# Kernel optimization log

Hardware: AMD Instinct MI355X
Metric: run time of the kernel (lower is better)

Reference implementation:

```python
import jax, jax.numpy as jnp
import numpy as np

N_NODES = 10000
N_EDGES = 320000
MUL = 32            # multiplicity of each irrep block (32x0e + 32x1o)
H = 4               # attention heads (divides MUL)
D_IN = MUL + 3 * MUL  # 128
N_BASIS = 8         # radial basis size (edge_scalar_attr dim)
HID = 64            # features=[64] hidden layer of the weight-MLP
INV3 = 1.0 / np.sqrt(3.0)  # CG normalization for 1o x 1o -> 0e


def _mlp(x, w1, b1, w2):
    # HTensorProductMLP weight net: edge scalars -> per-path uvu weights
    h = jax.nn.gelu(x @ w1 * (1.0 / np.sqrt(N_BASIS)) + b1)
    return (h @ w2) * (1.0 / np.sqrt(HID))  # (E, 4*MUL)


def _tp_uvu(w, xs, xv, ys, yv):
    # uvu tensor product of (32x0e+32x1o) x (1x0e+1x1o) keeping {0e,1o} outputs.
    # Sorted output blocks: [0e: s*s, 0e: v.v, 1o: s*v, 1o: v*s]
    w = w.reshape(-1, 4, MUL)
    o0 = w[:, 0] * xs * ys[:, None]                              # (E,MUL)
    o1 = w[:, 1] * jnp.einsum('eud,ed->eu', xv, yv) * INV3       # (E,MUL)
    o2 = w[:, 2][:, :, None] * xs[:, :, None] * yv[:, None, :]   # (E,MUL,3)
    o3 = w[:, 3][:, :, None] * xv * ys[:, None, None]            # (E,MUL,3)
    return o0, o1, o2, o3


def setup_inputs() -> dict:
    key = jax.random.key(0)
    ks = jax.random.split(key, 13)
    E, N = N_EDGES, N_NODES
    return {
        'edge_src': jax.random.randint(ks[0], (E,), 0, N, dtype=jnp.int32),
        'edge_dst': jax.random.randint(ks[1], (E,), 0, N, dtype=jnp.int32),
        'edge_scalar_attr': jax.random.uniform(ks[2], (E, N_BASIS), dtype=jnp.float32),
        'edge_attr': jax.random.normal(ks[3], (E, 4), dtype=jnp.float32),
        'edge_weight_cutoff': jax.random.uniform(ks[4], (E,), dtype=jnp.float32),
        'node_f': jax.random.normal(ks[5], (N, D_IN), dtype=jnp.float32),
        'wk1': jax.random.normal(ks[6], (N_BASIS, HID), dtype=jnp.float32),
        'bk1': jnp.zeros((HID,), jnp.float32),
        'wk2': jax.random.normal(ks[7], (HID, 4 * MUL), dtype=jnp.float32),
        'wv1': jax.random.normal(ks[8], (N_BASIS, HID), dtype=jnp.float32),
        'bv1': jnp.zeros((HID,), jnp.float32),
        'wv2': jax.random.normal(ks[9], (HID, 4 * MUL), dtype=jnp.float32),
        'W_dot': jax.random.normal(ks[10], (4, H, MUL, MUL), dtype=jnp.float32),
        'W_lin_s': jax.random.normal(ks[11], (2 * MUL, MUL), dtype=jnp.float32),
        'W_lin_v': jax.random.normal(ks[12], (2 * MUL, MUL), dtype=jnp.float32),
    }


def reference(edge_src, edge_dst, edge_scalar_attr, edge_attr, edge_weight_cutoff,
              node_f, wk1, bk1, wk2, wv1, bv1, wv2, W_dot, W_lin_s, W_lin_v):
    N = node_f.shape[0]
    xs = node_f[:, :MUL]                       # (N,MUL)   0e block
    xv = node_f[:, MUL:].reshape(N, MUL, 3)    # (N,MUL,3) 1o block
    ys = edge_attr[:, 0]                       # (E,)  Y_0
    yv = edge_attr[:, 1:4]                     # (E,3) Y_1
    sxs, sxv = xs[edge_src], xv[edge_src]      # gather source node feats

    # keys: per-edge equivariant tensor-product MLP
    wk = _mlp(edge_scalar_attr, wk1, bk1, wk2)
    k0, k1, kv0, kv1 = _tp_uvu(wk, sxs, sxv, ys, yv)

    # attention logits: fully-connected TP (dst node, key) -> Hx0e
    qs, qv = xs[edge_dst], xv[edge_dst]
    inv_fan = 1.0 / np.sqrt(4.0 * MUL * MUL)
    d = (jnp.einsum('huv,eu,ev->eh', W_dot[0], qs, k0)
         + jnp.einsum('huv,eu,ev->eh', W_dot[1], qs, k1)
         + jnp.einsum('huv,eud,evd->eh', W_dot[2], qv, kv0) * INV3
         + jnp.einsum('huv,eud,evd->eh', W_dot[3], qv, kv1) * INV3) * inv_fan
    expw = edge_weight_cutoff[:, None] * jnp.exp(d)              # (E,H)
    z = jax.ops.segment_sum(expw, edge_dst, num_segments=N)      # (N,H)
    z = jnp.where(z == 0.0, 1.0, z)
    alpha = expw / z[edge_dst]                                   # (E,H)

    # values: second per-edge equivariant tensor-product MLP
    wv = _mlp(edge_scalar_attr, wv1, bv1, wv2)
    v0, v1, vv0, vv1 = _tp_uvu(wv, sxs, sxv, ys, yv)
    sa = jnp.sqrt(jax.nn.relu(alpha))                            # (E,H)
    Ee = sa.shape[0]
    m = MUL // H
    e0 = (v0.reshape(Ee, H, m) * sa[:, :, None]).reshape(Ee, MUL)
    e1 = (v1.reshape(Ee, H, m) * sa[:, :, None]).reshape(Ee, MUL)
    e2 = (vv0.reshape(Ee, H, m, 3) * sa[:, :, None, None]).reshape(Ee, 3 * MUL)
    e3 = (vv1.reshape(Ee, H, m, 3) * sa[:, :, None, None]).reshape(Ee, 3 * MUL)
    edge_v = jnp.concatenate([e0, e1, e2, e3], axis=-1)          # (E, 8*MUL)

    agg = jax.ops.segment_sum(edge_v, edge_dst, num_segments=N)  # (N, 8*MUL)

    # equivariant HLinear: mix multiplicities within each irrep
    s = agg[:, :2 * MUL]                                         # (N,2*MUL)
    v = agg[:, 2 * MUL:].reshape(N, 2 * MUL, 3)                  # (N,2*MUL,3)
    inv_l = 1.0 / np.sqrt(2.0 * MUL)
    out_s = (s @ W_lin_s) * inv_l                                # (N,MUL)
    out_v = jnp.einsum('nud,uw->nwd', v, W_lin_v) * inv_l        # (N,MUL,3)
    return jnp.concatenate([out_s, out_v.reshape(N, 3 * MUL)], axis=-1)
```

## Files before the change

### kernel.cpp

```cpp
#include <hip/hip_runtime.h>


constexpr float INV3    = 0.57735026918962576f;
constexpr float INV_SQ8 = 0.35355339059327373f;
constexpr float INV_HID = 0.125f;
constexpr float INV_FAN = 0.015625f;
constexpr float INV_L   = 0.125f;
constexpr int   MAXD    = 128;

__device__ __forceinline__ float gelu_tanh(float x) {
  float u = 0.7978845608028654f * (x + 0.044715f * x * x * x);
  float e = __expf(2.0f * u);
  return x * (1.0f - 1.0f / (e + 1.0f));
}

__global__ void k_zero(int* __restrict__ p, int n) {
  int i = blockIdx.x * 256 + threadIdx.x;
  if (i < n) p[i] = 0;
}

__global__ void k_hist(const int* __restrict__ dst, int* __restrict__ cnt, int E) {
  int e = blockIdx.x * 256 + threadIdx.x;
  if (e < E) atomicAdd(&cnt[dst[e]], 1);
}

__global__ __launch_bounds__(256) void k_scan(const int* __restrict__ cnt,
                                              int* __restrict__ rowptr, int N) {
  __shared__ int wsum[4];
  __shared__ int woff[4];
  __shared__ int carry;
  int t = threadIdx.x, wave = t >> 6, lane = t & 63;
  if (t == 0) { carry = 0; rowptr[0] = 0; }
  __syncthreads();
  for (int base = 0; base < N; base += 256) {
    int i = base + t;
    int inc = (i < N) ? cnt[i] : 0;
#pragma unroll
    for (int off = 1; off < 64; off <<= 1) {
      int y = __shfl_up(inc, off, 64);
      if (lane >= off) inc += y;
    }
    if (lane == 63) wsum[wave] = inc;
    __syncthreads();
    if (t == 0) {
      int r = 0;
      for (int w = 0; w < 4; w++) { woff[w] = r; r += wsum[w]; }
    }
    __syncthreads();
    int incl = inc + woff[wave] + carry;
    if (i < N) rowptr[i + 1] = incl;
    __syncthreads();
    if (t == 255) carry = incl;
    __syncthreads();
  }
}

__global__ void k_fill(const int* __restrict__ dst, const int* __restrict__ rowptr,
                       int* __restrict__ cursor, int* __restrict__ csr, int E) {
  int e = blockIdx.x * 256 + threadIdx.x;
  if (e < E) {
    int d = dst[e];
    int s = atomicAdd(&cursor[d], 1);
    csr[rowptr[d] + s] = e;
  }
}

__global__ void k_dhist(const int* __restrict__ rowptr, int* __restrict__ dbin, int N) {
  int n = blockIdx.x * 256 + threadIdx.x;
  if (n < N) {
    int deg = rowptr[n + 1] - rowptr[n];
    atomicAdd(&dbin[min(deg, 127)], 1);
  }
}

__global__ void k_dscan(const int* __restrict__ dbin, int* __restrict__ doff) {
  if (threadIdx.x == 0 && blockIdx.x == 0) {
    int r = 0;
    for (int d = 127; d >= 0; --d) { doff[d] = r; r += dbin[d]; }
  }
}

__global__ void k_dfill(const int* __restrict__ rowptr, const int* __restrict__ doff,
                        int* __restrict__ dcur, int* __restrict__ nperm, int N) {
  int n = blockIdx.x * 256 + threadIdx.x;
  if (n < N) {
    int d = min(rowptr[n + 1] - rowptr[n], 127);
    int p = doff[d] + atomicAdd(&dcur[d], 1);
    nperm[p] = n;
  }
}

__global__ __launch_bounds__(256) void k_gather(
    const int* __restrict__ csr, const int* __restrict__ esrc,
    const float* __restrict__ xattr, const float* __restrict__ eattr,
    const float* __restrict__ cutoff,
    float* __restrict__ xc, float* __restrict__ ec, float* __restrict__ cc,
    int* __restrict__ srcc, int E) {
  int p = blockIdx.x * 256 + threadIdx.x;
  if (p >= E) return;
  int e = csr[p];
  srcc[p] = esrc[e];
  cc[p] = cutoff[e];
  ((float4*)ec)[p] = ((const float4*)eattr)[e];
  const float4* xs = (const float4*)xattr + (size_t)e * 2;
  float4* xd = (float4*)xc + (size_t)p * 2;
  xd[0] = xs[0]; xd[1] = xs[1];
}

__global__ __launch_bounds__(256) void k_nodeA(const float* __restrict__ node_f,
                                               const float* __restrict__ Wdot,
                                               float* __restrict__ A, int N) {
  __shared__ float Wd[16384];
  __shared__ float nfs[32 * 128];
  int t = threadIdx.x;
  for (int i = t; i < 16384; i += 256) Wd[i] = Wdot[i];
  int n0 = blockIdx.x * 32;
  int nEnd = min(32, N - n0);
  for (int i = t; i < nEnd * 128; i += 256) nfs[i] = node_f[n0 * 128 + i];
  __syncthreads();
  for (int nn = 0; nn < nEnd; ++nn) {
    const float* nf = &nfs[nn * 128];
    float* An = &A[(n0 + nn) * 1024];
#pragma unroll
    for (int k = 0; k < 4; k++) {
      int o = t + k * 256;
      float acc = 0.f;
      int idx;
      if (o < 256) {
        int term = o >> 7, h = (o >> 5) & 3, v = o & 31;
        const float* W = &Wd[term * 4096 + h * 1024 + v];
#pragma unroll
        for (int u = 0; u < 32; u++) acc += W[u * 32] * nf[u];
        idx = term * 128 + v * 4 + h;
      } else {
        int r = o - 256;
        int term = r / 384;
        int rr = r % 384;
        int h = rr / 96, q = rr % 96, v = q / 3, d = q - 3 * (q / 3);
        const float* W = &Wd[(term + 2) * 4096 + h * 1024 + v];
#pragma unroll
        for (int u = 0; u < 32; u++) acc += W[u * 32] * nf[32 + u * 3 + d];
        idx = 256 + term * 384 + v * 12 + h * 3 + d;
      }
      An[idx] = acc;
    }
  }
}

__global__ __launch_bounds__(256) void k_mlp(
    const float* __restrict__ xc,
    const float* __restrict__ w1, const float* __restrict__ b1,
    const float* __restrict__ w2,
    float* __restrict__ wm,
    int E, int chunk)
{
  __shared__ __align__(16) float w1s[512];
  __shared__ float b1s[64];
  __shared__ __align__(16) float wq[16][128][4];
  __shared__ __align__(16) float Hs[4][4][64];

  int t = threadIdx.x;
  int wave = t >> 6, lane = t & 63;
  for (int i = t; i < 512; i += 256) w1s[i] = w1[i];
  if (t < 64) b1s[t] = b1[t];
  for (int i = t; i < 8192; i += 256) {
    int l = i >> 7, j = i & 127;
    int js = j ^ ((j >> 3) & 7);
    wq[l >> 2][js][l & 3] = w2[i];
  }
  __syncthreads();

  int base = blockIdx.x * chunk;
  int end = min(base + chunk, E);
  int v = lane & 31;
  bool hi = lane >= 32;
  int c0 = lane, c1 = lane + 64;
  int c0s = c0 ^ ((c0 >> 3) & 7);
  int c1s = c1 ^ ((c1 >> 3) & 7);

  for (int sb = base + wave * 4; sb < end; sb += 16) {
    int sl[4];
#pragma unroll
    for (int k = 0; k < 4; k++) sl[k] = min(sb + k, E - 1);
    float h[4];
#pragma unroll
    for (int k = 0; k < 4; k++) {
      const float4* xp = (const float4*)xc + (size_t)sl[k] * 2;
      float4 xa = xp[0], xb = xp[1];
      float acc = xa.x * w1s[lane]       + xa.y * w1s[64 + lane]
                + xa.z * w1s[128 + lane] + xa.w * w1s[192 + lane]
                + xb.x * w1s[256 + lane] + xb.y * w1s[320 + lane]
                + xb.z * w1s[384 + lane] + xb.w * w1s[448 + lane];
      h[k] = gelu_tanh(acc * INV_SQ8 + b1s[lane]);
    }
#pragma unroll
    for (int k = 0; k < 4; k++) Hs[wave][k][lane] = h[k];
    float a0[4] = {0, 0, 0, 0}, a1[4] = {0, 0, 0, 0};
#pragma unroll
    for (int q = 0; q < 16; q++) {
      float4 wA = *(const float4*)&wq[q][c0s][0];
      float4 wB = *(const float4*)&wq[q][c1s][0];
#pragma unroll
      for (int k = 0; k < 4; k++) {
        float4 hq = *(const float4*)&Hs[wave][k][q * 4];
        a0[k] += hq.x * wA.x + hq.y * wA.y + hq.z * wA.z + hq.w * wA.w;
        a1[k] += hq.x * wB.x + hq.y * wB.y + hq.z * wB.z + hq.w * wB.w;
      }
    }
#pragma unroll
    for (int k = 0; k < 4; k++) {
      if (sb + k < end) {
        float2 o = make_float2(a0[k] * INV_HID, a1[k] * INV_HID);
        ((float2*)wm)[(size_t)sl[k] * 64 + (hi ? 32 : 0) + v] = o;
      }
    }
  }
}

__global__ __launch_bounds__(256) void k_att(
    const int* __restrict__ rowptr,
    const int* __restrict__ nperm,
    const int* __restrict__ srcc,
    const float* __restrict__ ec,
    const float* __restrict__ cc,
    const float* __restrict__ node_f,
    const float* __restrict__ wm,
    const float* __restrict__ A,
    float* __restrict__ sa_out,
    int N)
{
  __shared__ float expws[4][MAXD][4];

  int t = threadIdx.x;
  int wave = t >> 6, lane = t & 63;
  int idx = blockIdx.x * 4 + wave;
  if (idx >= N) return;
  int n = nperm[idx];
  int row0 = rowptr[n];
  int deg = min(rowptr[n + 1] - row0, MAXD);
  if (deg <= 0) return;

  int v = lane & 31;
  bool hi = lane >= 32;
  int kk = (lane >> 2) & 3;

  float aS[4], aV[12];
  {
    const float* Ab = A + (size_t)n * 1024;
    const float* ps = Ab + (hi ? 128 : 0) + v * 4;
    float4 t0 = *(const float4*)ps;
    aS[0] = t0.x; aS[1] = t0.y; aS[2] = t0.z; aS[3] = t0.w;
    const float* pv = Ab + (hi ? 640 : 256) + v * 12;
    float4 u0 = *(const float4*)pv;
    float4 u1 = *(const float4*)(pv + 4);
    float4 u2 = *(const float4*)(pv + 8);
    aV[0] = u0.x; aV[1] = u0.y; aV[2]  = u0.z; aV[3]  = u0.w;
    aV[4] = u1.x; aV[5] = u1.y; aV[6]  = u1.z; aV[7]  = u1.w;
    aV[8] = u2.x; aV[9] = u2.y; aV[10] = u2.z; aV[11] = u2.w;
  }

  int iters = (deg + 3) >> 2;
  float zacc = 0.f;

  for (int it = 0; it < iters; ++it) {
    int sb = it * 4;
    int slot[4]; int sp[4];
#pragma unroll
    for (int k = 0; k < 4; k++) slot[k] = row0 + min(sb + k, deg - 1);
#pragma unroll
    for (int k = 0; k < 4; k++) sp[k] = srcc[slot[k]];
    float4 ya[4]; float cf[4]; float2 wj[4]; float s0[4], s1[4], s2[4];
#pragma unroll
    for (int k = 0; k < 4; k++) {
      ya[k] = ((const float4*)ec)[slot[k]];
      cf[k] = (sb + k < deg) ? cc[slot[k]] : 0.f;
      wj[k] = ((const float2*)wm)[(size_t)slot[k] * 64 + (hi ? 32 : 0) + v];
      const float* nf = &node_f[(size_t)sp[k] * 128];
      if (!hi) { s0[k] = nf[v]; s1[k] = 0.f; s2[k] = 0.f; }
      else     { s0[k] = nf[32 + v * 3]; s1[k] = nf[33 + v * 3]; s2[k] = nf[34 + v * 3]; }
    }
    float p[16];
#pragma unroll
    for (int k = 0; k < 4; k++) {
      float ys = ya[k].x, yv0 = ya[k].y, yv1 = ya[k].z, yv2 = ya[k].w;
      if (!hi) {
        float k0 = wj[k].x * s0[k] * ys;
        float kb = INV3 * wj[k].y * s0[k];
#pragma unroll
        for (int h2 = 0; h2 < 4; h2++)
          p[k * 4 + h2] = aS[h2] * k0 +
              kb * (aV[h2 * 3] * yv0 + aV[h2 * 3 + 1] * yv1 + aV[h2 * 3 + 2] * yv2);
      } else {
        float dotv = s0[k] * yv0 + s1[k] * yv1 + s2[k] * yv2;
        float k1 = wj[k].x * dotv * INV3;
        float kc = INV3 * wj[k].y * ys;
#pragma unroll
        for (int h2 = 0; h2 < 4; h2++)
          p[k * 4 + h2] = aS[h2] * k1 +
              kc * (aV[h2 * 3] * s0[k] + aV[h2 * 3 + 1] * s1[k] + aV[h2 * 3 + 2] * s2[k]);
      }
    }
    bool fb0 = (lane & 1) != 0;
    float q8[8];
#pragma unroll
    for (int j = 0; j < 8; j++) {
      float a = p[2 * j], b = p[2 * j + 1];
      float keep = fb0 ? b : a, send = fb0 ? a : b;
      q8[j] = keep + __shfl_xor(send, 1, 64);
    }
    bool fb1 = (lane & 2) != 0;
    float r4[4];
#pragma unroll
    for (int j = 0; j < 4; j++) {
      float a = q8[2 * j], b = q8[2 * j + 1];
      float keep = fb1 ? b : a, send = fb1 ? a : b;
      r4[j] = keep + __shfl_xor(send, 2, 64);
    }
    bool fb2 = (lane & 4) != 0;
    float s2v[2];
#pragma unroll
    for (int j = 0; j < 2; j++) {
      float a = r4[2 * j], b = r4[2 * j + 1];
      float keep = fb2 ? b : a, send = fb2 ? a : b;
      s2v[j] = keep + __shfl_xor(send, 4, 64);
    }
    bool fb3 = (lane & 8) != 0;
    float w;
    {
      float a = s2v[0], b = s2v[1];
      float keep = fb3 ? b : a, send = fb3 ? a : b;
      w = keep + __shfl_xor(send, 8, 64);
    }
    w += __shfl_xor(w, 16, 64);
    w += __shfl_xor(w, 32, 64);
    float cA = (lane & 4) ? cf[1] : cf[0];
    float cB = (lane & 4) ? cf[3] : cf[2];
    float cfs = (lane & 8) ? cB : cA;
    int slotw = sb + kk;
    float ex = cfs * __expf(w * INV_FAN);
    if (lane < 16 && slotw < deg) {
      expws[wave][slotw][lane & 3] = ex;
      zacc += ex;
    }
  }
  float zr = zacc;
  zr += __shfl_xor(zr, 4, 64);
  zr += __shfl_xor(zr, 8, 64);
  float zf = __shfl(zr, lane & 3, 64);
  zf = (zf == 0.f) ? 1.f : zf;
  for (int i = lane; i < deg * 4; i += 64) {
    int slot = i >> 2;
    float alpha = expws[wave][slot][lane & 3] / zf;
    sa_out[(size_t)(row0 + slot) * 4 + (lane & 3)] = sqrtf(fmaxf(alpha, 0.f));
  }
}

__global__ __launch_bounds__(256) void k_agg(
    const int* __restrict__ rowptr,
    const int* __restrict__ nperm,
    const int* __restrict__ srcc,
    const float* __restrict__ ec,
    const float* __restrict__ node_f,
    const float* __restrict__ wm,
    const float* __restrict__ Wls, const float* __restrict__ Wlv,
    const float* __restrict__ sa_in,
    float* __restrict__ out,
    int N)
{
  __shared__ float aggv[4][256];

  int t = threadIdx.x;
  int wave = t >> 6, lane = t & 63;
  int idx = blockIdx.x * 4 + wave;
  if (idx >= N) return;
  int n = nperm[idx];
  int row0 = rowptr[n];
  int deg = min(rowptr[n + 1] - row0, MAXD);

  int v = lane & 31;
  bool hi = lane >= 32;
  int hh = v >> 3;
  float accS = 0.f, acc0 = 0.f, acc1 = 0.f, acc2 = 0.f;

  if (deg > 0) {
    int iters = (deg + 3) >> 2;
    for (int it = 0; it < iters; ++it) {
      int sb = it * 4;
      int slot[4]; int sp[4];
#pragma unroll
      for (int k = 0; k < 4; k++) slot[k] = row0 + min(sb + k, deg - 1);
#pragma unroll
      for (int k = 0; k < 4; k++) sp[k] = srcc[slot[k]];
      float4 ya[4]; float sav[4]; float2 wj[4]; float s0[4], s1[4], s2[4];
#pragma unroll
      for (int k = 0; k < 4; k++) {
        sav[k] = (sb + k < deg) ? sa_in[(size_t)slot[k] * 4 + hh] : 0.f;
        ya[k] = ((const float4*)ec)[slot[k]];
        wj[k] = ((const float2*)wm)[(size_t)slot[k] * 64 + (hi ? 32 : 0) + v];
        const float* nf = &node_f[(size_t)sp[k] * 128];
        if (!hi) { s0[k] = nf[v]; s1[k] = 0.f; s2[k] = 0.f; }
        else     { s0[k] = nf[32 + v * 3]; s1[k] = nf[33 + v * 3]; s2[k] = nf[34 + v * 3]; }
      }
#pragma unroll
      for (int k = 0; k < 4; k++) {
        float ys = ya[k].x, yv0 = ya[k].y, yv1 = ya[k].z, yv2 = ya[k].w;
        float sav_k = sav[k];
        if (!hi) {
          accS += wj[k].x * s0[k] * ys * sav_k;
          float b = wj[k].y * s0[k] * sav_k;
          acc0 += b * yv0; acc1 += b * yv1; acc2 += b * yv2;
        } else {
          float dotv = s0[k] * yv0 + s1[k] * yv1 + s2[k] * yv2;
          accS += wj[k].x * dotv * INV3 * sav_k;
          float c = wj[k].y * ys * sav_k;
          acc0 += c * s0[k]; acc1 += c * s1[k]; acc2 += c * s2[k];
        }
      }
    }
  }
  {
    int us = hi ? 32 + v : v;
    aggv[wave][us]       = accS;
    aggv[wave][64 + us]  = acc0;
    aggv[wave][128 + us] = acc1;
    aggv[wave][192 + us] = acc2;
    const float* agg = aggv[wave];
#pragma unroll
    for (int rep = 0; rep < 2; ++rep) {
      int o = lane + rep * 64;
      float acc = 0.f;
      if (o < 32) {
#pragma unroll
        for (int u = 0; u < 64; u++) acc += agg[u] * Wls[u * 32 + o];
      } else {
        int i = o - 32, w2 = i / 3, d = i - 3 * w2;
        const float* av = &agg[64 + d * 64];
#pragma unroll
        for (int u = 0; u < 64; u++) acc += av[u] * Wlv[u * 32 + w2];
      }
      out[(size_t)n * 128 + o] = acc * INV_L;
    }
  }
}

extern "C" void kernel_launch(void* const* d_in, const int* in_sizes, int n_in,
                              void* d_out, int out_size, void* d_ws, size_t ws_size,
                              hipStream_t stream) {
  const int*   esrc   = (const int*)d_in[0];
  const int*   edst   = (const int*)d_in[1];
  const float* xattr  = (const float*)d_in[2];
  const float* eattr  = (const float*)d_in[3];
  const float* cutoff = (const float*)d_in[4];
  const float* node_f = (const float*)d_in[5];
  const float* wk1    = (const float*)d_in[6];
  const float* bk1    = (const float*)d_in[7];
  const float* wk2    = (const float*)d_in[8];
  const float* wv1    = (const float*)d_in[9];
  const float* bv1    = (const float*)d_in[10];
  const float* wv2    = (const float*)d_in[11];
  const float* Wdot   = (const float*)d_in[12];
  const float* Wls    = (const float*)d_in[13];
  const float* Wlv    = (const float*)d_in[14];
  float* out = (float*)d_out;

  int E = in_sizes[0];
  int N = in_sizes[5] / 128;

  float* A    = (float*)d_ws;
  float* sa   = A + (size_t)N * 1024;
  float* xc   = sa + (size_t)E * 4;
  float* ec   = xc + (size_t)E * 8;
  float* cc   = ec + (size_t)E * 4;
  int* srcc   = (int*)(cc + (size_t)E);
  int* counts = srcc + E;
  int* cursor = counts + N;
  int* dbin   = cursor + N;
  int* dcur   = dbin + 128;
  int* rowptr = dcur + 128;
  int* doff   = rowptr + (N + 1);
  int* nperm  = doff + 128;
  int* csr    = nperm + N;
  float* wm   = (float*)(csr + E);

  k_zero<<<(2 * N + 256 + 255) / 256, 256, 0, stream>>>(counts, 2 * N + 256);
  k_hist<<<(E + 255) / 256, 256, 0, stream>>>(edst, counts, E);
  k_scan<<<1, 256, 0, stream>>>(counts, rowptr, N);
  k_fill<<<(E + 255) / 256, 256, 0, stream>>>(edst, rowptr, cursor, csr, E);
  k_dhist<<<(N + 255) / 256, 256, 0, stream>>>(rowptr, dbin, N);
  k_dscan<<<1, 64, 0, stream>>>(dbin, doff);
  k_dfill<<<(N + 255) / 256, 256, 0, stream>>>(rowptr, doff, dcur, nperm, N);
  k_gather<<<(E + 255) / 256, 256, 0, stream>>>(csr, esrc, xattr, eattr, cutoff,
                                                xc, ec, cc, srcc, E);
  k_nodeA<<<(N + 31) / 32, 256, 0, stream>>>(node_f, Wdot, A, N);

  int mgrid = 512;
  int chunk = (E + mgrid - 1) / mgrid;
  int nb = (N + 3) / 4;

  k_mlp<<<mgrid, 256, 0, stream>>>(xc, wk1, bk1, wk2, wm, E, chunk);
  k_att<<<nb, 256, 0, stream>>>(rowptr, nperm, srcc, ec, cc, node_f, wm, A, sa, N);
  k_mlp<<<mgrid, 256, 0, stream>>>(xc, wv1, bv1, wv2, wm, E, chunk);
  k_agg<<<nb, 256, 0, stream>>>(rowptr, nperm, srcc, ec, node_f, wm,
                                Wls, Wlv, sa, out, N);
}
```

Baseline: 875.3 us.

## Run value-MLP and attention concurrently in one horizontally fused launch

Splits the MLP and attention kernels into device-function bodies and adds a combined kernel. Its first mgrid blocks compute the value-path MLP weights into a separate buffer while the remaining blocks compute attention from the key-path weights. This removes a serialization point so the two independent stages can overlap on the GPU. The cost is a second E×128 weight buffer, used only when the workspace is large enough, and a larger combined shared-memory footprint per block that may reduce occupancy.

```diff
diff --git a/kernel.cpp b/kernel.cpp
--- a/kernel.cpp
+++ b/kernel.cpp
@@ -147,18 +147,12 @@
   }
 }
 
-__global__ __launch_bounds__(256) void k_mlp(
+__device__ __forceinline__ void mlp_body(
     const float* __restrict__ xc,
     const float* __restrict__ w1, const float* __restrict__ b1,
     const float* __restrict__ w2,
-    float* __restrict__ wm,
-    int E, int chunk)
-{
-  __shared__ __align__(16) float w1s[512];
-  __shared__ float b1s[64];
-  __shared__ __align__(16) float wq[16][128][4];
-  __shared__ __align__(16) float Hs[4][4][64];
-
+    float* __restrict__ wm, int E, int chunk, int blk,
+    float* w1s, float* b1s, float (*wq)[128][4], float (*Hs)[4][64]) {
   int t = threadIdx.x;
   int wave = t >> 6, lane = t & 63;
   for (int i = t; i < 512; i += 256) w1s[i] = w1[i];
@@ -170,7 +164,7 @@
   }
   __syncthreads();
 
-  int base = blockIdx.x * chunk;
+  int base = blk * chunk;
   int end = min(base + chunk, E);
   int v = lane & 31;
   bool hi = lane >= 32;
@@ -217,23 +211,16 @@
   }
 }
 
-__global__ __launch_bounds__(256) void k_att(
-    const int* __restrict__ rowptr,
-    const int* __restrict__ nperm,
-    const int* __restrict__ srcc,
-    const float* __restrict__ ec,
-    const float* __restrict__ cc,
-    const float* __restrict__ node_f,
-    const float* __restrict__ wm,
-    const float* __restrict__ A,
-    float* __restrict__ sa_out,
-    int N)
-{
-  __shared__ float expws[4][MAXD][4];
-
+__device__ __forceinline__ void att_body(
+    const int* __restrict__ rowptr, const int* __restrict__ nperm,
+    const int* __restrict__ srcc, const float* __restrict__ ec,
+    const float* __restrict__ cc, const float* __restrict__ node_f,
+    const float* __restrict__ wm, const float* __restrict__ A,
+    float* __restrict__ sa_out, int N, int blk,
+    float (*expws)[MAXD][4]) {
   int t = threadIdx.x;
   int wave = t >> 6, lane = t & 63;
-  int idx = blockIdx.x * 4 + wave;
+  int idx = blk * 4 + wave;
   if (idx >= N) return;
   int n = nperm[idx];
   int row0 = rowptr[n];
@@ -352,6 +339,52 @@
     int slot = i >> 2;
     float alpha = expws[wave][slot][lane & 3] / zf;
     sa_out[(size_t)(row0 + slot) * 4 + (lane & 3)] = sqrtf(fmaxf(alpha, 0.f));
+  }
+}
+
+__global__ __launch_bounds__(256) void k_mlp(
+    const float* __restrict__ xc,
+    const float* __restrict__ w1, const float* __restrict__ b1,
+    const float* __restrict__ w2,
+    float* __restrict__ wm, int E, int chunk) {
+  __shared__ __align__(16) float w1s[512];
+  __shared__ float b1s[64];
+  __shared__ __align__(16) float wq[16][128][4];
+  __shared__ __align__(16) float Hs[4][4][64];
+  mlp_body(xc, w1, b1, w2, wm, E, chunk, blockIdx.x, w1s, b1s, wq, Hs);
+}
+
+__global__ __launch_bounds__(256) void k_att(
+    const int* __restrict__ rowptr, const int* __restrict__ nperm,
+    const int* __restrict__ srcc, const float* __restrict__ ec,
+    const float* __restrict__ cc, const float* __restrict__ node_f,
+    const float* __restrict__ wm, const float* __restrict__ A,
+    float* __restrict__ sa_out, int N) {
+  __shared__ float expws[4][MAXD][4];
+  att_body(rowptr, nperm, srcc, ec, cc, node_f, wm, A, sa_out, N,
+           blockIdx.x, expws);
+}
+
+__global__ __launch_bounds__(256) void k_mva(
+    const float* __restrict__ xc,
+    const float* __restrict__ wv1, const float* __restrict__ bv1,
+    const float* __restrict__ wv2,
+    float* __restrict__ wmV, int E, int chunk, int mgrid,
+    const int* __restrict__ rowptr, const int* __restrict__ nperm,
+    const int* __restrict__ srcc, const float* __restrict__ ec,
+    const float* __restrict__ cc, const float* __restrict__ node_f,
+    const float* __restrict__ wmK, const float* __restrict__ A,
+    float* __restrict__ sa_out, int N) {
+  __shared__ __align__(16) float w1s[512];
+  __shared__ float b1s[64];
+  __shared__ __align__(16) float wq[16][128][4];
+  __shared__ __align__(16) float Hs[4][4][64];
+  __shared__ float expws[4][MAXD][4];
+  if ((int)blockIdx.x < mgrid) {
+    mlp_body(xc, wv1, bv1, wv2, wmV, E, chunk, blockIdx.x, w1s, b1s, wq, Hs);
+  } else {
+    att_body(rowptr, nperm, srcc, ec, cc, node_f, wmK, A, sa_out, N,
+             blockIdx.x - mgrid, expws);
   }
 }
 
@@ -480,7 +513,12 @@
   int* doff   = rowptr + (N + 1);
   int* nperm  = doff + 128;
   int* csr    = nperm + N;
-  float* wm   = (float*)(csr + E);
+  float* wmK  = (float*)(csr + E);
+  float* wmV  = wmK + (size_t)E * 128;
+
+  size_t need_fused = (size_t)((char*)(wmV + (size_t)E * 128) - (char*)d_ws);
+  bool fused = ws_size >= need_fused;
+  if (!fused) wmV = wmK;
 
   k_zero<<<(2 * N + 256 + 255) / 256, 256, 0, stream>>>(counts, 2 * N + 256);
   k_hist<<<(E + 255) / 256, 256, 0, stream>>>(edst, counts, E);
@@ -497,9 +535,16 @@
   int chunk = (E + mgrid - 1) / mgrid;
   int nb = (N + 3) / 4;
 
-  k_mlp<<<mgrid, 256, 0, stream>>>(xc, wk1, bk1, wk2, wm, E, chunk);
-  k_att<<<nb, 256, 0, stream>>>(rowptr, nperm, srcc, ec, cc, node_f, wm, A, sa, N);
-  k_mlp<<<mgrid, 256, 0, stream>>>(xc, wv1, bv1, wv2, wm, E, chunk);
-  k_agg<<<nb, 256, 0, stream>>>(rowptr, nperm, srcc, ec, node_f, wm,
+  k_mlp<<<mgrid, 256, 0, stream>>>(xc, wk1, bk1, wk2, wmK, E, chunk);
+  if (fused) {
+    k_mva<<<mgrid + nb, 256, 0, stream>>>(xc, wv1, bv1, wv2, wmV, E, chunk,
+                                          mgrid, rowptr, nperm, srcc, ec, cc,
+                                          node_f, wmK, A, sa, N);
+  } else {
+    k_att<<<nb, 256, 0, stream>>>(rowptr, nperm, srcc, ec, cc, node_f,
+                                  wmK, A, sa, N);
+    k_mlp<<<mgrid, 256, 0, stream>>>(xc, wv1, bv1, wv2, wmV, E, chunk);
+  }
+  k_agg<<<nb, 256, 0, stream>>>(rowptr, nperm, srcc, ec, node_f, wmV,
                                 Wls, Wlv, sa, out, N);
 }
```

New measurement: 866.6 us. About the same (-1.0%).
